# Optimization experiments

Measured on AMD Instinct MI355X. Metric: run time of the kernel, lower is better.

## Reference

```python
import jax, jax.numpy as jnp
import numpy as np

T, D, H, E, K = 4096, 1024, 2816, 8, 2


def setup_inputs() -> dict:
    key = jax.random.key(0)
    ks = jax.random.split(key, 5)
    s = 0.02
    return {
        "x": jax.random.normal(ks[0], (T, D), dtype=jnp.float32),
        "gate_w": jax.random.normal(ks[1], (D, E), dtype=jnp.float32) * s,
        "w1": jax.random.normal(ks[2], (E, D, H), dtype=jnp.float32) * s,
        "w2": jax.random.normal(ks[3], (E, H, D), dtype=jnp.float32) * s,
        "w3": jax.random.normal(ks[4], (E, D, H), dtype=jnp.float32) * s,
    }


def reference(x, gate_w, w1, w2, w3):
    # gate + top-k routing
    gate_logits = x @ gate_w                          # [T, E]
    topk_vals, sel = jax.lax.top_k(gate_logits, K)    # [T, K]
    topk_w = jax.nn.softmax(topk_vals.astype(jnp.float32), axis=-1).astype(x.dtype)
    # scatter top-k weights back to a dense [T, E] combine matrix
    tok = jnp.arange(x.shape[0])[:, None]             # [T, 1]
    combine = jnp.zeros(gate_logits.shape, x.dtype).at[tok, sel].set(topk_w)  # [T, E]
    # per-expert SwiGLU FFN, evaluated densely and combined with (mostly-zero) weights;
    # mathematically identical to the masked gather/scatter loop in the original.
    h = jax.nn.silu(jnp.einsum("td,edh->teh", x, w1)) * jnp.einsum("td,edh->teh", x, w3)
    expert_out = jnp.einsum("teh,ehd->ted", h, w2)    # [T, E, D]
    return jnp.einsum("ted,te->td", expert_out, combine)
```

## Files before the change

### kernel.cpp

```cpp
#include <hip/hip_runtime.h>
#include <hip/hip_bf16.h>
#include <cstdint>
#include <cstddef>


#define Tt 4096
#define Dd 1024
#define Hh 2816
#define Ee 8
#define NVT 71

typedef __bf16 bf16_t;
typedef __bf16 bf16x4 __attribute__((ext_vector_type(4)));
typedef __bf16 bf16x8 __attribute__((ext_vector_type(8)));
typedef float f32x4 __attribute__((ext_vector_type(4)));

__device__ __forceinline__ void gload16(const void* g, void* l) {
  __builtin_amdgcn_global_load_lds(
      (__attribute__((address_space(1))) void*)(void*)(uintptr_t)g,
      (__attribute__((address_space(3))) void*)l, 16, 0, 0);
}
#define WAIT_VM0() asm volatile("s_waitcnt vmcnt(0)" ::: "memory")

__global__ __launch_bounds__(256) void gate_kernel(
    const float* __restrict__ x, const float* __restrict__ gw_g,
    int* __restrict__ counts, int* __restrict__ perm, float* __restrict__ topkw,
    bf16_t* __restrict__ xb) {
  __shared__ float gw[Dd * 9];
  const int tid = threadIdx.x;
  for (int i = tid; i < Dd * Ee; i += 256) gw[(i >> 3) * 9 + (i & 7)] = gw_g[i];
  __syncthreads();
  const int tok = blockIdx.x * 32 + (tid >> 3);
  const int part = tid & 7;
  const float* xr = x + (size_t)tok * Dd;
  float acc[Ee];
#pragma unroll
  for (int e = 0; e < Ee; ++e) acc[e] = 0.f;
  for (int i = 0; i < 32; ++i) {
    const int d = i * 32 + part * 4;
    const float4 xv = *(const float4*)(xr + d);
    bf16x4 bv; bv[0] = (__bf16)xv.x; bv[1] = (__bf16)xv.y; bv[2] = (__bf16)xv.z; bv[3] = (__bf16)xv.w;
    *(bf16x4*)(xb + (size_t)tok * Dd + d) = bv;
    const float xs[4] = {xv.x, xv.y, xv.z, xv.w};
#pragma unroll
    for (int j = 0; j < 4; ++j)
#pragma unroll
      for (int e = 0; e < Ee; ++e) acc[e] += xs[j] * gw[(d + j) * 9 + e];
  }
#pragma unroll
  for (int s = 1; s < 8; s <<= 1)
#pragma unroll
    for (int e = 0; e < Ee; ++e) acc[e] += __shfl_xor(acc[e], s, 64);
  if (part == 0) {
    int i0 = 0; float v0 = acc[0];
#pragma unroll
    for (int e = 1; e < Ee; ++e) if (acc[e] > v0) { v0 = acc[e]; i0 = e; }
    int i1 = -1; float v1 = -1e30f;
#pragma unroll
    for (int e = 0; e < Ee; ++e)
      if (e != i0 && acc[e] > v1) { v1 = acc[e]; i1 = e; }
    const float w0 = 1.f / (1.f + __expf(v1 - v0));
    topkw[tok * 2 + 0] = w0;
    topkw[tok * 2 + 1] = 1.f - w0;
    const int p0 = atomicAdd(&counts[i0], 1);
    perm[i0 * Tt + p0] = tok * 2 + 0;
    const int p1 = atomicAdd(&counts[i1], 1);
    perm[i1 * Tt + p1] = tok * 2 + 1;
  }
}

__global__ void scan_kernel(const int* __restrict__ counts, int* __restrict__ offs,
                            int* __restrict__ ts) {
  if (threadIdx.x == 0) {
    int s = 0, t = 0;
    for (int e = 0; e < Ee; ++e) {
      offs[e] = s; ts[e] = t;
      s += counts[e]; t += (counts[e] + 127) >> 7;
    }
    offs[Ee] = s; ts[Ee] = t;
  }
}

__global__ __launch_bounds__(256) void prep_w_kernel(
    const float* __restrict__ w1, const float* __restrict__ w3,
    const float* __restrict__ w2, bf16_t* __restrict__ w1t,
    bf16_t* __restrict__ w3t, bf16_t* __restrict__ w2t) {
  int bid = blockIdx.x;
  const int ntile = Ee * (Dd / 64) * (Hh / 64);
  const float* src; bf16_t* dst; int R, C;
  if (bid < ntile) { src = w1; dst = w1t; R = Dd; C = Hh; }
  else if (bid < 2 * ntile) { src = w3; dst = w3t; R = Dd; C = Hh; bid -= ntile; }
  else { src = w2; dst = w2t; R = Hh; C = Dd; bid -= 2 * ntile; }
  const int tilesC = C / 64, tilesR = R / 64;
  const int e = bid / (tilesR * tilesC);
  const int rem = bid % (tilesR * tilesC);
  const int r0 = (rem / tilesC) * 64, c0 = (rem % tilesC) * 64;
  src += (size_t)e * R * C;
  dst += (size_t)e * R * C;

  __shared__ bf16_t tile[64 * 68];
  const int tid = threadIdx.x;
  const int rr0 = tid >> 4;
  const int c4 = (tid & 15) * 4;
#pragma unroll
  for (int i = 0; i < 4; ++i) {
    const int r = rr0 + i * 16;
    const float4 v = *(const float4*)(src + (size_t)(r0 + r) * C + c0 + c4);
    tile[(c4 + 0) * 68 + r] = (__bf16)v.x;
    tile[(c4 + 1) * 68 + r] = (__bf16)v.y;
    tile[(c4 + 2) * 68 + r] = (__bf16)v.z;
    tile[(c4 + 3) * 68 + r] = (__bf16)v.w;
  }
  __syncthreads();
  const int rch = (tid & 7) * 8;
#pragma unroll
  for (int i = 0; i < 2; ++i) {
    const int c = (tid >> 3) + i * 32;
    const uint2 lo = *(const uint2*)(tile + c * 68 + rch);
    const uint2 hi = *(const uint2*)(tile + c * 68 + rch + 4);
    uint4 val; val.x = lo.x; val.y = lo.y; val.z = hi.x; val.w = hi.y;
    *(uint4*)(dst + (size_t)(c0 + c) * R + r0 + rch) = val;
  }
}

__global__ __launch_bounds__(256, 2) void ffn1_kernel(
    const bf16_t* __restrict__ xb, const bf16_t* __restrict__ w1t,
    const bf16_t* __restrict__ w3t, const int* __restrict__ perm,
    const int* __restrict__ counts, const int* __restrict__ offs,
    const int* __restrict__ ts, bf16_t* __restrict__ hbuf) {
  const int G = (Hh / 128) * NVT;
  const int orig = blockIdx.x;
  const int xcd = orig & 7, seq = orig >> 3;
  const int q = G >> 3, r = G & 7;
  const int lin = (xcd < r ? xcd * (q + 1) : r * (q + 1) + (xcd - r) * q) + seq;
  const int vt = lin % NVT;
  const int nb = lin / NVT;
  if (vt >= ts[Ee]) return;
  int e = 0;
#pragma unroll
  for (int i = 1; i < Ee; ++i) if (vt >= ts[i]) e = i;
  const int ne = counts[e];
  const int m0 = (vt - ts[e]) * 128;
  const int h0 = nb * 128;
  const int hb = offs[e];

  __shared__ __align__(16) bf16_t As[128 * 64];
  __shared__ __align__(16) bf16_t B1s[128 * 64];
  __shared__ __align__(16) bf16_t B3s[128 * 64];

  const int tid = threadIdx.x;
  const int lane = tid & 63;
  const int wid = tid >> 6;

  const int scol = ((tid & 7) << 3) ^ (((tid >> 3) & 7) << 3);
  uint32_t aoff[4], boff[4];
#pragma unroll
  for (int i = 0; i < 4; ++i) {
    const int row = i * 32 + (tid >> 3);
    const int gr = m0 + row;
    const int rec = (gr < ne) ? perm[e * Tt + gr] : 0;
    aoff[i] = (uint32_t)((rec >> 1) * Dd + scol);
    boff[i] = (uint32_t)((h0 + row) * Dd + scol);
  }
  const bf16_t* w1e = w1t + (size_t)e * Hh * Dd;
  const bf16_t* w3e = w3t + (size_t)e * Hh * Dd;

  f32x4 acc1[4][4], acc3[4][4];
#pragma unroll
  for (int m = 0; m < 4; ++m)
#pragma unroll
    for (int n = 0; n < 4; ++n) {
      acc1[m][n] = (f32x4){0.f, 0.f, 0.f, 0.f};
      acc3[m][n] = (f32x4){0.f, 0.f, 0.f, 0.f};
    }

  const int wm = wid >> 1, wn = wid & 1;
  int aoffm[4], boffn[4], koff[2];
#pragma unroll
  for (int m = 0; m < 4; ++m) aoffm[m] = (wm * 64 + m * 16 + (lane & 15)) * 64;
#pragma unroll
  for (int n = 0; n < 4; ++n) boffn[n] = (wn * 64 + n * 16 + (lane & 15)) * 64;
#pragma unroll
  for (int kk = 0; kk < 2; ++kk)
    koff[kk] = (kk * 32 + (lane >> 4) * 8) ^ ((lane & 7) << 3);

  for (int kt = 0; kt < Dd / 64; ++kt) {
    const int d0 = kt * 64;
    __syncthreads();
#pragma unroll
    for (int i = 0; i < 4; ++i) {
      const int lb = (i * 256 + tid) * 8;
      gload16(xb + aoff[i] + d0, As + lb);
      gload16(w1e + boff[i] + d0, B1s + lb);
      gload16(w3e + boff[i] + d0, B3s + lb);
    }
    WAIT_VM0();
    __syncthreads();
#pragma unroll
    for (int kk = 0; kk < 2; ++kk) {
      bf16x8 a[4], b1[4], b3[4];
#pragma unroll
      for (int m = 0; m < 4; ++m) a[m] = *(const bf16x8*)(As + aoffm[m] + koff[kk]);
#pragma unroll
      for (int n = 0; n < 4; ++n) {
        b1[n] = *(const bf16x8*)(B1s + boffn[n] + koff[kk]);
        b3[n] = *(const bf16x8*)(B3s + boffn[n] + koff[kk]);
      }
#pragma unroll
      for (int m = 0; m < 4; ++m)
#pragma unroll
        for (int n = 0; n < 4; ++n) {
          acc1[m][n] = __builtin_amdgcn_mfma_f32_16x16x32_bf16(a[m], b1[n], acc1[m][n], 0, 0, 0);
          acc3[m][n] = __builtin_amdgcn_mfma_f32_16x16x32_bf16(a[m], b3[n], acc3[m][n], 0, 0, 0);
        }
    }
  }

#pragma unroll
  for (int m = 0; m < 4; ++m) {
    const int rb = m0 + wm * 64 + m * 16 + ((lane >> 4) << 2);
#pragma unroll
    for (int r2 = 0; r2 < 4; ++r2) {
      const int gr = rb + r2;
      if (gr >= ne) continue;
      bf16_t* orow = hbuf + (size_t)(hb + gr) * Hh + h0 + wn * 64 + (lane & 15);
#pragma unroll
      for (int n = 0; n < 4; ++n) {
        const float v1 = acc1[m][n][r2];
        const float v3 = acc3[m][n][r2];
        const float s = v1 / (1.f + __expf(-v1));
        orow[n * 16] = (__bf16)(s * v3);
      }
    }
  }
}

__global__ __launch_bounds__(256, 3) void ffn2_kernel(
    const bf16_t* __restrict__ hbuf, const bf16_t* __restrict__ w2t,
    const int* __restrict__ perm, const int* __restrict__ counts,
    const int* __restrict__ offs, const int* __restrict__ ts,
    const float* __restrict__ topkw, float* __restrict__ obuf) {
  const int G = (Dd / 128) * NVT;
  const int orig = blockIdx.x;
  const int xcd = orig & 7, seq = orig >> 3;
  const int q = G >> 3, r = G & 7;
  const int lin = (xcd < r ? xcd * (q + 1) : r * (q + 1) + (xcd - r) * q) + seq;
  const int vt = lin % NVT;
  const int nb = lin / NVT;
  if (vt >= ts[Ee]) return;
  int e = 0;
#pragma unroll
  for (int i = 1; i < Ee; ++i) if (vt >= ts[i]) e = i;
  const int ne = counts[e];
  const int m0 = (vt - ts[e]) * 128;
  const int n0 = nb * 128;
  const int hb = offs[e];

  __shared__ __align__(16) bf16_t As[128 * 64];
  __shared__ __align__(16) bf16_t Bs[128 * 64];

  const int tid = threadIdx.x;
  const int lane = tid & 63;
  const int wid = tid >> 6;
  const int scol = ((tid & 7) << 3) ^ (((tid >> 3) & 7) << 3);
  uint32_t aoff[4], boff[4];
#pragma unroll
  for (int i = 0; i < 4; ++i) {
    const int row = i * 32 + (tid >> 3);
    int ar = hb + m0 + row;
    if (ar > 2 * Tt - 1) ar = 2 * Tt - 1;
    aoff[i] = (uint32_t)(ar * Hh + scol);
    boff[i] = (uint32_t)((n0 + row) * Hh + scol);
  }
  const bf16_t* w2e = w2t + (size_t)e * Dd * Hh;

  f32x4 acc[4][4];
#pragma unroll
  for (int m = 0; m < 4; ++m)
#pragma unroll
    for (int n = 0; n < 4; ++n) acc[m][n] = (f32x4){0.f, 0.f, 0.f, 0.f};

  const int wm = wid >> 1, wn = wid & 1;
  int aoffm[4], boffn[4], koff[2];
#pragma unroll
  for (int m = 0; m < 4; ++m) aoffm[m] = (wm * 64 + m * 16 + (lane & 15)) * 64;
#pragma unroll
  for (int n = 0; n < 4; ++n) boffn[n] = (wn * 64 + n * 16 + (lane & 15)) * 64;
#pragma unroll
  for (int kk = 0; kk < 2; ++kk)
    koff[kk] = (kk * 32 + (lane >> 4) * 8) ^ ((lane & 7) << 3);

  for (int kt = 0; kt < Hh / 64; ++kt) {
    const int k0 = kt * 64;
    __syncthreads();
#pragma unroll
    for (int i = 0; i < 4; ++i) {
      const int lb = (i * 256 + tid) * 8;
      gload16(hbuf + aoff[i] + k0, As + lb);
      gload16(w2e + boff[i] + k0, Bs + lb);
    }
    WAIT_VM0();
    __syncthreads();
#pragma unroll
    for (int kk = 0; kk < 2; ++kk) {
      bf16x8 a[4], b[4];
#pragma unroll
      for (int m = 0; m < 4; ++m) a[m] = *(const bf16x8*)(As + aoffm[m] + koff[kk]);
#pragma unroll
      for (int n = 0; n < 4; ++n) b[n] = *(const bf16x8*)(Bs + boffn[n] + koff[kk]);
#pragma unroll
      for (int m = 0; m < 4; ++m)
#pragma unroll
        for (int n = 0; n < 4; ++n)
          acc[m][n] = __builtin_amdgcn_mfma_f32_16x16x32_bf16(a[m], b[n], acc[m][n], 0, 0, 0);
    }
  }

#pragma unroll
  for (int m = 0; m < 4; ++m) {
    const int rb = m0 + wm * 64 + m * 16 + ((lane >> 4) << 2);
#pragma unroll
    for (int r2 = 0; r2 < 4; ++r2) {
      const int gr = rb + r2;
      if (gr >= ne) continue;
      const int rec = perm[e * Tt + gr];
      const float wgt = topkw[rec];
      float* orow = obuf + (size_t)rec * Dd + n0 + wn * 64 + (lane & 15);
#pragma unroll
      for (int n = 0; n < 4; ++n) orow[n * 16] = wgt * acc[m][n][r2];
    }
  }
}

__global__ __launch_bounds__(256) void combine_kernel(const float* __restrict__ obuf,
                                                      float* __restrict__ out) {
  const int t = blockIdx.x;
  const int d = threadIdx.x * 4;
  const float4 a = *(const float4*)(obuf + (size_t)(2 * t) * Dd + d);
  const float4 b = *(const float4*)(obuf + (size_t)(2 * t + 1) * Dd + d);
  float4 o;
  o.x = a.x + b.x; o.y = a.y + b.y; o.z = a.z + b.z; o.w = a.w + b.w;
  *(float4*)(out + (size_t)t * Dd + d) = o;
}

extern "C" void kernel_launch(void* const* d_in, const int* in_sizes, int n_in,
                              void* d_out, int out_size, void* d_ws, size_t ws_size,
                              hipStream_t stream) {
  const float* x = (const float*)d_in[0];
  const float* gate_w = (const float*)d_in[1];
  const float* w1 = (const float*)d_in[2];
  const float* w2 = (const float*)d_in[3];
  const float* w3 = (const float*)d_in[4];
  float* out = (float*)d_out;

  char* ws = (char*)d_ws;
  size_t off = 0;
  auto alloc = [&](size_t b) { size_t r = off; off += (b + 255) & ~(size_t)255; return r; };
  float* topkw   = (float*)(ws + alloc((size_t)Tt * 2 * 4));
  int* counts    = (int*)(ws + alloc(Ee * 4));
  int* offs      = (int*)(ws + alloc((Ee + 1) * 4));
  int* ts        = (int*)(ws + alloc((Ee + 1) * 4));
  int* perm      = (int*)(ws + alloc((size_t)Ee * Tt * 4));
  bf16_t* xb     = (bf16_t*)(ws + alloc((size_t)Tt * Dd * 2));
  const size_t w1t_off = alloc((size_t)Ee * Hh * Dd * 2);
  bf16_t* w1t    = (bf16_t*)(ws + w1t_off);
  bf16_t* w3t    = (bf16_t*)(ws + alloc((size_t)Ee * Hh * Dd * 2));
  bf16_t* w2t    = (bf16_t*)(ws + alloc((size_t)Ee * Dd * Hh * 2));
  bf16_t* hbuf   = (bf16_t*)(ws + alloc((size_t)Tt * 2 * Hh * 2));
  float* obuf    = (float*)(ws + w1t_off);
  if (ws_size < off) return;

  hipMemsetAsync(counts, 0, Ee * 4, stream);
  gate_kernel<<<Tt / 32, 256, 0, stream>>>(x, gate_w, counts, perm, topkw, xb);
  scan_kernel<<<1, 64, 0, stream>>>(counts, offs, ts);
  prep_w_kernel<<<3 * Ee * (Dd / 64) * (Hh / 64), 256, 0, stream>>>(w1, w3, w2, w1t, w3t, w2t);
  ffn1_kernel<<<(Hh / 128) * NVT, 256, 0, stream>>>(xb, w1t, w3t, perm, counts, offs, ts, hbuf);
  ffn2_kernel<<<(Dd / 128) * NVT, 256, 0, stream>>>(hbuf, w2t, perm, counts, offs, ts, topkw, obuf);
  combine_kernel<<<Tt, 256, 0, stream>>>(obuf, out);
}
```

Baseline: 333.7 us.

## Fuse weight conversion into gate and ffn1 kernels to overlap prep work

The standalone weight transpose/convert kernel is removed. The w1/w3 conversion blocks are appended to the gate kernel's grid, and the w2 conversion blocks are appended to the ffn1 grid, so prep work runs alongside the gating and the first GEMM instead of in its own launch. This saves launches and lets the memory-bound conversion overlap compute. In exchange, the w2 prep blocks share the ffn1 grid and its launch bounds and LDS allocation, which may lower occupancy, and scheduling depends on the order in which blocks are dispatched.

After: 294.6 us. 11.7% less time.

```diff
diff --git a/kernel.cpp b/kernel.cpp
--- a/kernel.cpp
+++ b/kernel.cpp
@@ -9,6 +9,8 @@
 #define Hh 2816
 #define Ee 8
 #define NVT 71
+#define NTILE 5632
+#define FFN1_BLKS ((Hh / 128) * NVT)
 
 typedef __bf16 bf16_t;
 typedef __bf16 bf16x4 __attribute__((ext_vector_type(4)));
@@ -22,15 +24,57 @@
 }
 #define WAIT_VM0() asm volatile("s_waitcnt vmcnt(0)" ::: "memory")
 
-__global__ __launch_bounds__(256) void gate_kernel(
+__device__ __forceinline__ void prep_tile(const float* __restrict__ src,
+                                          bf16_t* __restrict__ dst, int R, int C,
+                                          int tbid, bf16_t* tile, int tid) {
+  const int tilesC = C / 64, tilesR = R / 64;
+  const int e = tbid / (tilesR * tilesC);
+  const int rem = tbid % (tilesR * tilesC);
+  const int r0 = (rem / tilesC) * 64, c0 = (rem % tilesC) * 64;
+  src += (size_t)e * R * C;
+  dst += (size_t)e * R * C;
+  const int rr0 = tid >> 4;
+  const int c4 = (tid & 15) * 4;
+#pragma unroll
+  for (int i = 0; i < 4; ++i) {
+    const int r = rr0 + i * 16;
+    const float4 v = *(const float4*)(src + (size_t)(r0 + r) * C + c0 + c4);
+    tile[(c4 + 0) * 68 + r] = (__bf16)v.x;
+    tile[(c4 + 1) * 68 + r] = (__bf16)v.y;
+    tile[(c4 + 2) * 68 + r] = (__bf16)v.z;
+    tile[(c4 + 3) * 68 + r] = (__bf16)v.w;
+  }
+  __syncthreads();
+  const int rch = (tid & 7) * 8;
+#pragma unroll
+  for (int i = 0; i < 2; ++i) {
+    const int c = (tid >> 3) + i * 32;
+    const uint2 lo = *(const uint2*)(tile + c * 68 + rch);
+    const uint2 hi = *(const uint2*)(tile + c * 68 + rch + 4);
+    uint4 val; val.x = lo.x; val.y = lo.y; val.z = hi.x; val.w = hi.y;
+    *(uint4*)(dst + (size_t)(c0 + c) * R + r0 + rch) = val;
+  }
+}
+
+__global__ __launch_bounds__(256) void gate_prep13_kernel(
     const float* __restrict__ x, const float* __restrict__ gw_g,
+    const float* __restrict__ w1, const float* __restrict__ w3,
     int* __restrict__ counts, int* __restrict__ perm, float* __restrict__ topkw,
-    bf16_t* __restrict__ xb) {
-  __shared__ float gw[Dd * 9];
+    bf16_t* __restrict__ xb, bf16_t* __restrict__ w1t, bf16_t* __restrict__ w3t) {
+  __shared__ __align__(16) char smem[Dd * 9 * 4];
   const int tid = threadIdx.x;
+  const int bid = blockIdx.x;
+  if (bid >= 128) {
+    const int pbid = bid - 128;
+    bf16_t* tile = (bf16_t*)smem;
+    if (pbid < NTILE) prep_tile(w1, w1t, Dd, Hh, pbid, tile, tid);
+    else prep_tile(w3, w3t, Dd, Hh, pbid - NTILE, tile, tid);
+    return;
+  }
+  float* gw = (float*)smem;
   for (int i = tid; i < Dd * Ee; i += 256) gw[(i >> 3) * 9 + (i & 7)] = gw_g[i];
   __syncthreads();
-  const int tok = blockIdx.x * 32 + (tid >> 3);
+  const int tok = bid * 32 + (tid >> 3);
   const int part = tid & 7;
   const float* xr = x + (size_t)tok * Dd;
   float acc[Ee];
@@ -81,56 +125,25 @@
   }
 }
 
-__global__ __launch_bounds__(256) void prep_w_kernel(
-    const float* __restrict__ w1, const float* __restrict__ w3,
-    const float* __restrict__ w2, bf16_t* __restrict__ w1t,
-    bf16_t* __restrict__ w3t, bf16_t* __restrict__ w2t) {
-  int bid = blockIdx.x;
-  const int ntile = Ee * (Dd / 64) * (Hh / 64);
-  const float* src; bf16_t* dst; int R, C;
-  if (bid < ntile) { src = w1; dst = w1t; R = Dd; C = Hh; }
-  else if (bid < 2 * ntile) { src = w3; dst = w3t; R = Dd; C = Hh; bid -= ntile; }
-  else { src = w2; dst = w2t; R = Hh; C = Dd; bid -= 2 * ntile; }
-  const int tilesC = C / 64, tilesR = R / 64;
-  const int e = bid / (tilesR * tilesC);
-  const int rem = bid % (tilesR * tilesC);
-  const int r0 = (rem / tilesC) * 64, c0 = (rem % tilesC) * 64;
-  src += (size_t)e * R * C;
-  dst += (size_t)e * R * C;
-
-  __shared__ bf16_t tile[64 * 68];
+__global__ __launch_bounds__(256, 2) void ffn1_prep2_kernel(
+    const bf16_t* __restrict__ xb, const bf16_t* __restrict__ w1t,
+    const bf16_t* __restrict__ w3t, const float* __restrict__ w2,
+    const int* __restrict__ perm, const int* __restrict__ counts,
+    const int* __restrict__ offs, const int* __restrict__ ts,
+    bf16_t* __restrict__ hbuf, bf16_t* __restrict__ w2t) {
+  __shared__ __align__(16) char smem[3 * 128 * 64 * 2];
   const int tid = threadIdx.x;
-  const int rr0 = tid >> 4;
-  const int c4 = (tid & 15) * 4;
-#pragma unroll
-  for (int i = 0; i < 4; ++i) {
-    const int r = rr0 + i * 16;
-    const float4 v = *(const float4*)(src + (size_t)(r0 + r) * C + c0 + c4);
-    tile[(c4 + 0) * 68 + r] = (__bf16)v.x;
-    tile[(c4 + 1) * 68 + r] = (__bf16)v.y;
-    tile[(c4 + 2) * 68 + r] = (__bf16)v.z;
-    tile[(c4 + 3) * 68 + r] = (__bf16)v.w;
-  }
-  __syncthreads();
-  const int rch = (tid & 7) * 8;
-#pragma unroll
-  for (int i = 0; i < 2; ++i) {
-    const int c = (tid >> 3) + i * 32;
-    const uint2 lo = *(const uint2*)(tile + c * 68 + rch);
-    const uint2 hi = *(const uint2*)(tile + c * 68 + rch + 4);
-    uint4 val; val.x = lo.x; val.y = lo.y; val.z = hi.x; val.w = hi.y;
-    *(uint4*)(dst + (size_t)(c0 + c) * R + r0 + rch) = val;
-  }
-}
-
-__global__ __launch_bounds__(256, 2) void ffn1_kernel(
-    const bf16_t* __restrict__ xb, const bf16_t* __restrict__ w1t,
-    const bf16_t* __restrict__ w3t, const int* __restrict__ perm,
-    const int* __restrict__ counts, const int* __restrict__ offs,
-    const int* __restrict__ ts, bf16_t* __restrict__ hbuf) {
-  const int G = (Hh / 128) * NVT;
-  const int orig = blockIdx.x;
-  const int xcd = orig & 7, seq = orig >> 3;
+  const int obid = blockIdx.x;
+  if (obid >= FFN1_BLKS) {
+    prep_tile(w2, w2t, Hh, Dd, obid - FFN1_BLKS, (bf16_t*)smem, tid);
+    return;
+  }
+  bf16_t* As = (bf16_t*)smem;
+  bf16_t* B1s = As + 128 * 64;
+  bf16_t* B3s = B1s + 128 * 64;
+
+  const int G = FFN1_BLKS;
+  const int xcd = obid & 7, seq = obid >> 3;
   const int q = G >> 3, r = G & 7;
   const int lin = (xcd < r ? xcd * (q + 1) : r * (q + 1) + (xcd - r) * q) + seq;
   const int vt = lin % NVT;
@@ -144,11 +157,6 @@
   const int h0 = nb * 128;
   const int hb = offs[e];
 
-  __shared__ __align__(16) bf16_t As[128 * 64];
-  __shared__ __align__(16) bf16_t B1s[128 * 64];
-  __shared__ __align__(16) bf16_t B3s[128 * 64];
-
-  const int tid = threadIdx.x;
   const int lane = tid & 63;
   const int wid = tid >> 6;
 
@@ -371,10 +379,11 @@
   if (ws_size < off) return;
 
   hipMemsetAsync(counts, 0, Ee * 4, stream);
-  gate_kernel<<<Tt / 32, 256, 0, stream>>>(x, gate_w, counts, perm, topkw, xb);
+  gate_prep13_kernel<<<128 + 2 * NTILE, 256, 0, stream>>>(
+      x, gate_w, w1, w3, counts, perm, topkw, xb, w1t, w3t);
   scan_kernel<<<1, 64, 0, stream>>>(counts, offs, ts);
-  prep_w_kernel<<<3 * Ee * (Dd / 64) * (Hh / 64), 256, 0, stream>>>(w1, w3, w2, w1t, w3t, w2t);
-  ffn1_kernel<<<(Hh / 128) * NVT, 256, 0, stream>>>(xb, w1t, w3t, perm, counts, offs, ts, hbuf);
+  ffn1_prep2_kernel<<<FFN1_BLKS + NTILE, 256, 0, stream>>>(
+      xb, w1t, w3t, w2, perm, counts, offs, ts, hbuf, w2t);
   ffn2_kernel<<<(Dd / 128) * NVT, 256, 0, stream>>>(hbuf, w2t, perm, counts, offs, ts, topkw, obuf);
   combine_kernel<<<Tt, 256, 0, stream>>>(obuf, out);
 }
```
